# Optimization experiments

Measured on AMD Instinct MI355X. Metric: run time of the kernel, lower is better.

The kernel has to match this reference:

```python
import jax, jax.numpy as jnp
import numpy as np

B, T, C = 4, 2048, 1024
H, D = 16, 64  # n_head, head_dim; H*D == C
EPS = 1e-12


def _l2norm(x):
    # matches torch F.normalize(dim=-1): x / max(||x||_2, eps)
    n = jnp.sqrt(jnp.sum(x * x, axis=-1, keepdims=True))
    return x / jnp.maximum(n, EPS)


def setup_inputs() -> dict:
    key = jax.random.key(0)
    ks = jax.random.split(key, 8)
    s = 0.02
    return {
        "x": jax.random.normal(ks[0], (B, T, C), dtype=jnp.float32),
        "Wq": jax.random.normal(ks[1], (C, C), dtype=jnp.float32) * s,
        "Wk": jax.random.normal(ks[2], (C, C), dtype=jnp.float32) * s,
        "Wv": jax.random.normal(ks[3], (C, C), dtype=jnp.float32) * s,
        "Wbeta": jax.random.normal(ks[4], (H, C), dtype=jnp.float32) * s,
        "bbeta": jnp.zeros((H,), dtype=jnp.float32),
        "Wgate": jax.random.normal(ks[5], (C, C), dtype=jnp.float32) * s,
        "Wo": jax.random.normal(ks[6], (C, C), dtype=jnp.float32) * s,
    }


def _forward(x, Wq, Wk, Wv, Wbeta, bbeta, Wgate, Wo):
    q = (x @ Wq.T).reshape(B, T, H, D)
    k = (x @ Wk.T).reshape(B, T, H, D)
    v = (x @ Wv.T).reshape(B, T, H, D)
    beta = jax.nn.sigmoid(x @ Wbeta.T + bbeta)  # (B,T,H)
    gate = jax.nn.sigmoid(x @ Wgate.T)          # (B,T,C)

    q = _l2norm(q)
    k = _l2norm(k)

    # time-major for scan: (T,B,H,D) / (T,B,H)
    qT = jnp.transpose(q, (1, 0, 2, 3))
    kT = jnp.transpose(k, (1, 0, 2, 3))
    vT = jnp.transpose(v, (1, 0, 2, 3))
    bT = jnp.transpose(beta, (1, 0, 2))

    M0 = jnp.zeros((B, H, D, D), dtype=x.dtype)

    def step(M, inp):
        q_t, k_t, v_t, b_t = inp
        o_t = jnp.einsum('bhdc,bhc->bhd', M, q_t)       # read state with q (pre-update)
        Mk = jnp.einsum('bhdc,bhc->bhd', M, k_t)
        dv = v_t - Mk                                    # delta-rule error
        M = M + b_t[..., None, None] * jnp.einsum('bhd,bhc->bhdc', dv, k_t)
        return M, o_t

    _, oT = jax.lax.scan(step, M0, (qT, kT, vT, bT))     # oT: (T,B,H,D)
    o = jnp.transpose(oT, (1, 0, 2, 3)).reshape(B, T, C)
    return (gate * o) @ Wo.T


def reference(x, Wq, Wk, Wv, Wbeta, bbeta, Wgate, Wo):
    return _forward(x, Wq, Wk, Wv, Wbeta, bbeta, Wgate, Wo)
```

## Files before the change

kernel.cpp:

```cpp
#include <hip/hip_runtime.h>
#include <cstdint>
#include <cstddef>

#define Bz 4
#define Tz 2048
#define Cz 1024
#define Hz 16
#define Dz 64
#define NTOK (Bz*Tz)
#define CHL 32
#define NCH (Tz/CHL)

typedef __attribute__((ext_vector_type(8))) short  short8;
typedef __attribute__((ext_vector_type(4))) float  floatx4;

__device__ __forceinline__ unsigned short f2bf(float x) {
  union { float f; uint32_t u; } a; a.f = x;
  uint32_t r = a.u + 0x7fffu + ((a.u >> 16) & 1u);
  return (unsigned short)(r >> 16);
}
__device__ __forceinline__ float bf2f(unsigned short u) {
  union { uint32_t i; float f; } a; a.i = ((uint32_t)u) << 16; return a.f;
}
__device__ __forceinline__ float sigmoidf_(float z) {
  return 1.0f / (1.0f + __expf(-z));
}

__device__ __forceinline__ void gload_lds16(const void* gptr, void* lptr) {
  __builtin_amdgcn_global_load_lds(
      (const __attribute__((address_space(1))) void*)(uintptr_t)gptr,
      (__attribute__((address_space(3))) void*)(uint32_t)(uintptr_t)lptr,
      16, 0, 0);
}

template<int CTRL>
__device__ __forceinline__ float dpp_addf(float x) {
  int y = __builtin_amdgcn_update_dpp(0, __float_as_int(x), CTRL, 0xF, 0xF, true);
  return x + __int_as_float(y);
}
__device__ __forceinline__ float rowsum16(float x) {
  x = dpp_addf<0xB1>(x);
  x = dpp_addf<0x4E>(x);
  x = dpp_addf<0x124>(x);
  x = dpp_addf<0x128>(x);
  return x;
}

union FragU { uint32_t u[4]; short8 s; };

__global__ __launch_bounds__(256) void cvt_bf16_kernel(const float* __restrict__ in,
                                                       unsigned short* __restrict__ out,
                                                       int n4) {
  int i = blockIdx.x * blockDim.x + threadIdx.x;
  int stride = gridDim.x * blockDim.x;
  const float4* in4 = (const float4*)in;
  ushort4* out4 = (ushort4*)out;
  for (; i < n4; i += stride) {
    float4 f = in4[i];
    ushort4 u;
    u.x = f2bf(f.x); u.y = f2bf(f.y); u.z = f2bf(f.z); u.w = f2bf(f.w);
    out4[i] = u;
  }
}

__global__ __launch_bounds__(256) void cvt_w5_kernel(
    const float* __restrict__ s0, const float* __restrict__ s1,
    const float* __restrict__ s2, const float* __restrict__ s3,
    const float* __restrict__ s4,
    unsigned short* __restrict__ d0, unsigned short* __restrict__ d1,
    unsigned short* __restrict__ d2, unsigned short* __restrict__ d3,
    unsigned short* __restrict__ d4, int n4)
{
  const int w = blockIdx.y;
  const float* s = (w == 0) ? s0 : (w == 1) ? s1 : (w == 2) ? s2 : (w == 3) ? s3 : s4;
  unsigned short* d = (w == 0) ? d0 : (w == 1) ? d1 : (w == 2) ? d2 : (w == 3) ? d3 : d4;
  int i = blockIdx.x * blockDim.x + threadIdx.x;
  if (i < n4) {
    float4 f = ((const float4*)s)[i];
    ushort4 u;
    u.x = f2bf(f.x); u.y = f2bf(f.y); u.z = f2bf(f.z); u.w = f2bf(f.w);
    ((ushort4*)d)[i] = u;
  }
}


#define VM8()  asm volatile("s_waitcnt vmcnt(8)" ::: "memory")
#define VM4()  asm volatile("s_waitcnt vmcnt(4)" ::: "memory")
#define VM0()  asm volatile("s_waitcnt vmcnt(0)" ::: "memory")
#define LGKM0() asm volatile("s_waitcnt lgkmcnt(0)" ::: "memory")
#define BARR() __builtin_amdgcn_s_barrier()

__global__ __launch_bounds__(512, 2) void gemm256_kernel(
    const unsigned short* __restrict__ A,
    const unsigned short* __restrict__ W0, const unsigned short* __restrict__ W1,
    const unsigned short* __restrict__ W2, const unsigned short* __restrict__ W3,
    void* __restrict__ O0, void* __restrict__ O1,
    void* __restrict__ O2, void* __restrict__ O3,
    int M, int N, int K, int nz_sigmoid, int norm_mask, int out_bf16)
{
  __shared__ unsigned short smem[8 * 8192];

  const int gx = gridDim.x, gz = gridDim.z;
  const int nwg = gx * gridDim.y * gz;
  int flat = (blockIdx.z * gridDim.y + blockIdx.y) * gx + blockIdx.x;
  if ((nwg & 7) == 0) flat = (flat & 7) * (nwg >> 3) + (flat >> 3);
  const int xz = gx * gz;
  const int by = flat / xz;
  const int rem = flat - by * xz;
  const int bz = rem / gx;
  const int bx = rem - bz * gx;

  const unsigned short* Bw = (bz == 0) ? W0 : (bz == 1) ? W1 : (bz == 2) ? W2 : W3;
  void* Cw = (bz == 0) ? O0 : (bz == 1) ? O1 : (bz == 2) ? O2 : O3;
  const bool act = (bz == nz_sigmoid);
  const bool donorm = (norm_mask >> bz) & 1;

  const int m0 = by * 256, n0 = bx * 256;
  const int tid = threadIdx.x;
  const int wid = tid >> 6, lane = tid & 63;
  const int wm = wid >> 2, wn = wid & 3;
  const int ml = lane & 15, kq = lane >> 4;

  const unsigned short* Ap = A  + (size_t)m0 * K;
  const unsigned short* Bp = Bw + (size_t)n0 * K;

  const int srow = wid * 16 + (lane >> 2);
  const int ss8  = ((lane & 3) ^ ((lane >> 3) & 3)) * 8;

  const int rs8  = (kq ^ ((ml >> 1) & 3)) * 8;
  const int arow = wm * 128 + ml;
  const int brow = wn * 64 + ml;

  const int NT = K >> 6;
  const int hmax = NT << 2;

  floatx4 acc[8][4];
#pragma unroll
  for (int i = 0; i < 8; ++i)
#pragma unroll
    for (int j = 0; j < 4; ++j) acc[i][j] = floatx4{0.f, 0.f, 0.f, 0.f};

#define STAGE1(hsi) do {                                                      \
    const int ht_ = (hsi) >> 2, hh_ = (hsi) & 3;                              \
    const unsigned short* p_ = (hh_ & 1) ? Bp : Ap;                           \
    const int kb_ = ht_ * 64 + (hh_ >> 1) * 32;                               \
    unsigned short* lb_ = &smem[(((ht_ & 1) << 2) + hh_) * 8192 + wid * 512]; \
    gload_lds16(p_ + (size_t)srow * K + kb_ + ss8, lb_);                      \
    gload_lds16(p_ + (size_t)(128 + srow) * K + kb_ + ss8, lb_ + 4096);       \
  } while (0)

  int hs = 0;
  for (; hs < 6 && hs < hmax; ++hs) STAGE1(hs);
  VM8();
  BARR();

#define LOAD_A(Hb, mh)                                                        \
  _Pragma("unroll") for (int i = 0; i < 4; ++i)                               \
    af[i] = *(const short8*)&Hb[(arow + (mh) * 64 + i * 16) * 32 + rs8];
#define LOAD_B(Hb)                                                            \
  _Pragma("unroll") for (int j = 0; j < 4; ++j)                               \
    bf[j] = *(const short8*)&Hb[(brow + j * 16) * 32 + rs8];
#define MFMA_Q(mh)                                                            \
  __builtin_amdgcn_s_setprio(1);                                              \
  _Pragma("unroll") for (int i = 0; i < 4; ++i)                               \
    _Pragma("unroll") for (int j = 0; j < 4; ++j)                             \
      acc[(mh) * 4 + i][j] = __builtin_amdgcn_mfma_f32_16x16x32_bf16(         \
          af[i], bf[j], acc[(mh) * 4 + i][j], 0, 0, 0);                       \
  __builtin_amdgcn_s_setprio(0);
#define STAGE_NEXT() do { if (hs < hmax) { STAGE1(hs); ++hs; } } while (0)

  short8 af[4], bf[4];
  for (int t = 0; t < NT; ++t) {
    const unsigned short* Ah0 = &smem[(((t & 1) << 2) + 0) * 8192];
    const unsigned short* Bh0 = &smem[(((t & 1) << 2) + 1) * 8192];
    const unsigned short* Ah1 = &smem[(((t & 1) << 2) + 2) * 8192];
    const unsigned short* Bh1 = &smem[(((t & 1) << 2) + 3) * 8192];

    LOAD_A(Ah0, 0); LOAD_B(Bh0);
    STAGE_NEXT();
    BARR(); LGKM0();
    MFMA_Q(0);
    BARR();

    LOAD_A(Ah0, 1);
    STAGE_NEXT();
    BARR(); LGKM0();
    MFMA_Q(1);
    if (t == NT - 1) { VM0(); } else { VM8(); }
    BARR();

    LOAD_A(Ah1, 0); LOAD_B(Bh1);
    STAGE_NEXT();
    BARR(); LGKM0();
    MFMA_Q(0);
    BARR();

    LOAD_A(Ah1, 1);
    STAGE_NEXT();
    BARR(); LGKM0();
    MFMA_Q(1);
    if (t < NT - 2) { VM8(); } else if (t == NT - 2) { VM4(); }
    BARR();
  }

  float scale[8][4];
  if (donorm) {
#pragma unroll
    for (int i = 0; i < 8; ++i) {
#pragma unroll
      for (int r = 0; r < 4; ++r) {
        float ss = 0.f;
#pragma unroll
        for (int j = 0; j < 4; ++j) ss = fmaf(acc[i][j][r], acc[i][j][r], ss);
        ss = rowsum16(ss);
        scale[i][r] = 1.0f / fmaxf(sqrtf(ss), 1e-12f);
      }
    }
  }

  const int row_base = m0 + wm * 128;
  const int col_base = n0 + wn * 64;
#pragma unroll
  for (int i = 0; i < 8; ++i) {
#pragma unroll
    for (int j = 0; j < 4; ++j) {
      const int col = col_base + j * 16 + ml;
#pragma unroll
      for (int r = 0; r < 4; ++r) {
        const int row = row_base + i * 16 + kq * 4 + r;
        float val = acc[i][j][r];
        if (donorm) val *= scale[i][r];
        if (act) val = sigmoidf_(val);
        if (out_bf16) ((unsigned short*)Cw)[(size_t)row * N + col] = f2bf(val);
        else          ((float*)Cw)[(size_t)row * N + col] = val;
      }
    }
  }
}

__global__ __launch_bounds__(256) void beta_kernel(
    const float* __restrict__ x, const float* __restrict__ Wb,
    const float* __restrict__ bb, float* __restrict__ beta_out)
{
  const int n = blockIdx.x;
  const int wid = threadIdx.x >> 6;
  const int lane = threadIdx.x & 63;
  const float* xr = x + (size_t)n * Cz;
  for (int h = wid; h < Hz; h += 4) {
    const float* wr = Wb + (size_t)h * Cz;
    float s = 0.f;
#pragma unroll 4
    for (int i = lane; i < Cz; i += 64) s = fmaf(xr[i], wr[i], s);
#pragma unroll
    for (int ofs = 32; ofs >= 1; ofs >>= 1) s += __shfl_xor(s, ofs);
    if (lane == 0) beta_out[(size_t)n * Hz + h] = sigmoidf_(s + bb[h]);
  }
}

__global__ __launch_bounds__(256) void deltachunk_phase1(
    const unsigned short* __restrict__ qb, const unsigned short* __restrict__ kb,
    const unsigned short* __restrict__ vb, const float* __restrict__ betaf,
    float* __restrict__ of,
    unsigned short* __restrict__ qtb, unsigned short* __restrict__ wbuf,
    unsigned short* __restrict__ ubuf, unsigned short* __restrict__ ktb)
{
  __shared__ unsigned short Kb[32][72], Qb[32][72], Vb[32][72];
  __shared__ float As[32][33];
  __shared__ unsigned short Sb[32][40];
  __shared__ unsigned short Us[32][72], Ws[32][72], Qts[32][72];
  __shared__ float bsh[32];

  const int bid = blockIdx.x;
  const int chain = bid & 63;
  const int chunk = bid >> 6;
  const int b = chain >> 4, h = chain & 15;
  const int tid = threadIdx.x;
  const int wid = tid >> 6, lane = tid & 63;
  const int ml = lane & 15, kq = lane >> 4;

  const size_t tok0 = (size_t)b * Tz + (size_t)chunk * CHL;
  const size_t cb = ((size_t)chain * NCH + chunk) * 2048;

  {
    const int row = tid >> 3, c8 = (tid & 7) * 8;
    const size_t ga = (tok0 + row) * Cz + h * Dz + c8;
    *(uint4*)&Qb[row][c8] = *(const uint4*)&qb[ga];
    *(uint4*)&Kb[row][c8] = *(const uint4*)&kb[ga];
    *(uint4*)&Vb[row][c8] = *(const uint4*)&vb[ga];
  }
  if (tid < 32) bsh[tid] = betaf[(tok0 + tid) * Hz + h];
  __syncthreads();

  {
    const int tr = wid & 1, tc = wid >> 1;
    floatx4 accA = {0.f,0.f,0.f,0.f}, accS = {0.f,0.f,0.f,0.f};
#pragma unroll
    for (int eh = 0; eh < 2; ++eh) {
      short8 ka = *(const short8*)&Kb[tr * 16 + ml][eh * 32 + kq * 8];
      short8 kbf = *(const short8*)&Kb[tc * 16 + ml][eh * 32 + kq * 8];
      short8 qa = *(const short8*)&Qb[tr * 16 + ml][eh * 32 + kq * 8];
      accA = __builtin_amdgcn_mfma_f32_16x16x32_bf16(ka, kbf, accA, 0, 0, 0);
      accS = __builtin_amdgcn_mfma_f32_16x16x32_bf16(qa, kbf, accS, 0, 0, 0);
    }
#pragma unroll
    for (int r = 0; r < 4; ++r) {
      int t = tr * 16 + kq * 4 + r;
      int s = tc * 16 + ml;
      As[t][s] = bsh[t] * accA[r];
      Sb[t][s] = (t > s) ? f2bf(accS[r]) : (unsigned short)0;
    }
  }
  __syncthreads();

  if (tid < 128) {
    const int j = tid;
    float x[32];
    if (j < 64) {
#pragma unroll
      for (int t = 0; t < 32; ++t) x[t] = bsh[t] * bf2f(Vb[t][j]);
    } else {
#pragma unroll
      for (int t = 0; t < 32; ++t) x[t] = bsh[t] * bf2f(Kb[t][j - 64]);
    }
#pragma unroll
    for (int t = 0; t < 31; ++t) {
      float xt = x[t];
#pragma unroll
      for (int s = t + 1; s < 32; ++s) x[s] = fmaf(-As[s][t], xt, x[s]);
    }
    if (j < 64) {
#pragma unroll
      for (int t = 0; t < 32; ++t) Us[t][j] = f2bf(x[t]);
    } else {
#pragma unroll
      for (int t = 0; t < 32; ++t) Ws[t][j - 64] = f2bf(x[t]);
    }
  }
  __syncthreads();

  {
    const int dw = wid * 16 + ml;
    FragU bu, bw;
#pragma unroll
    for (int r = 0; r < 4; ++r) {
      bu.u[r] = (uint32_t)Us[kq * 8 + 2 * r][dw] | ((uint32_t)Us[kq * 8 + 2 * r + 1][dw] << 16);
      bw.u[r] = (uint32_t)Ws[kq * 8 + 2 * r][dw] | ((uint32_t)Ws[kq * 8 + 2 * r + 1][dw] << 16);
    }
    floatx4 accO[2], accQ[2];
#pragma unroll
    for (int tt = 0; tt < 2; ++tt) { accO[tt] = floatx4{0.f,0.f,0.f,0.f}; accQ[tt] = floatx4{0.f,0.f,0.f,0.f}; }
#pragma unroll
    for (int tt = 0; tt < 2; ++tt) {
      short8 sa = *(const short8*)&Sb[tt * 16 + ml][kq * 8];
      accO[tt] = __builtin_amdgcn_mfma_f32_16x16x32_bf16(sa, bu.s, accO[tt], 0, 0, 0);
      accQ[tt] = __builtin_amdgcn_mfma_f32_16x16x32_bf16(sa, bw.s, accQ[tt], 0, 0, 0);
    }
#pragma unroll
    for (int tt = 0; tt < 2; ++tt) {
#pragma unroll
      for (int r = 0; r < 4; ++r) {
        int t = tt * 16 + kq * 4 + r;
        of[(tok0 + t) * Cz + h * Dz + dw] = accO[tt][r];
        Qts[t][dw] = f2bf(bf2f(Qb[t][dw]) - accQ[tt][r]);
      }
    }
  }

  unsigned short ktmp[8];
  {
    const int e = tid >> 2, tq = (tid & 3) * 8;
#pragma unroll
    for (int i2 = 0; i2 < 8; ++i2) ktmp[i2] = Kb[tq + i2][e];
  }
  __syncthreads();

  {
    const int row = tid >> 3, c8 = (tid & 7) * 8;
    const size_t o16 = cb + (size_t)row * 64 + c8;
    *(uint4*)&qtb[o16]  = *(const uint4*)&Qts[row][c8];
    *(uint4*)&wbuf[o16] = *(const uint4*)&Ws[row][c8];
    *(uint4*)&ubuf[o16] = *(const uint4*)&Us[row][c8];
    const int e = tid >> 2, tq = (tid & 3) * 8;
    *(uint4*)&ktb[cb + (size_t)e * 32 + tq] = *(const uint4*)ktmp;
  }
}

__global__ __launch_bounds__(256) void deltachunk_phase2(
    const unsigned short* __restrict__ qtb, const unsigned short* __restrict__ wbuf,
    const unsigned short* __restrict__ ubuf, const unsigned short* __restrict__ ktb,
    float* __restrict__ of)
{
  __shared__ unsigned short Gb[64][72];
  __shared__ unsigned short Kts[64][40];
  __shared__ unsigned short Ub[32][72];
  __shared__ unsigned short Mh[64][72], Ml[64][72];
  __shared__ unsigned short Zh[64][40], Zl[64][40];

  const int chain = blockIdx.x;
  const int b = chain >> 4, h = chain & 15;
  const int tid = threadIdx.x;
  const int wid = tid >> 6, lane = tid & 63;
  const int ml = lane & 15, kq = lane >> 4;
  const int iq = wid >> 1, jq = wid & 1;
  const int dq = wid >> 1, eq = wid & 1;

  for (int i = tid; i < 64 * 72; i += 256) { (&Mh[0][0])[i] = 0; (&Ml[0][0])[i] = 0; }
  floatx4 mAcc[2][2];
#pragma unroll
  for (int a = 0; a < 2; ++a)
#pragma unroll
    for (int e = 0; e < 2; ++e) mAcc[a][e] = floatx4{0.f,0.f,0.f,0.f};

  const int grow = tid >> 3, gc8 = (tid & 7) * 8;
  const int ke = tid >> 2,  kt8 = (tid & 3) * 8;

  {
    const size_t cb = (size_t)chain * NCH * 2048;
    *(uint4*)&Gb[grow][gc8]      = *(const uint4*)&qtb[cb + (size_t)grow * 64 + gc8];
    *(uint4*)&Gb[32 + grow][gc8] = *(const uint4*)&wbuf[cb + (size_t)grow * 64 + gc8];
    *(uint4*)&Ub[grow][gc8]      = *(const uint4*)&ubuf[cb + (size_t)grow * 64 + gc8];
    *(uint4*)&Kts[ke][kt8]       = *(const uint4*)&ktb[cb + (size_t)ke * 32 + kt8];
  }
  __syncthreads();

  for (int c = 0; c < NCH; ++c) {
    const size_t tok0 = (size_t)b * Tz + (size_t)c * CHL;
    float pre[2][2][4];
    if (iq == 0) {
#pragma unroll
      for (int ti = 0; ti < 2; ++ti)
#pragma unroll
        for (int tj = 0; tj < 2; ++tj)
#pragma unroll
          for (int r = 0; r < 4; ++r)
            pre[ti][tj][r] = of[(tok0 + ti * 16 + kq * 4 + r) * Cz + h * Dz + jq * 32 + tj * 16 + ml];
    }
    const int cn = (c + 1 < NCH) ? c + 1 : c;
    const size_t cbn = ((size_t)chain * NCH + cn) * 2048;
    uint4 sq = *(const uint4*)&qtb[cbn + (size_t)grow * 64 + gc8];
    uint4 sw = *(const uint4*)&wbuf[cbn + (size_t)grow * 64 + gc8];
    uint4 su = *(const uint4*)&ubuf[cbn + (size_t)grow * 64 + gc8];
    uint4 sk = *(const uint4*)&ktb[cbn + (size_t)ke * 32 + kt8];

    __syncthreads();

    floatx4 g1[2][2];
#pragma unroll
    for (int ti = 0; ti < 2; ++ti)
#pragma unroll
      for (int tj = 0; tj < 2; ++tj) g1[ti][tj] = floatx4{0.f,0.f,0.f,0.f};
#pragma unroll
    for (int eh = 0; eh < 2; ++eh) {
      short8 afr[2];
      afr[0] = *(const short8*)&Gb[iq * 32 + 0  + ml][eh * 32 + kq * 8];
      afr[1] = *(const short8*)&Gb[iq * 32 + 16 + ml][eh * 32 + kq * 8];
#pragma unroll
      for (int hl = 0; hl < 2; ++hl) {
#pragma unroll
        for (int tj = 0; tj < 2; ++tj) {
          short8 bfr = hl ? *(const short8*)&Ml[jq * 32 + tj * 16 + ml][eh * 32 + kq * 8]
                          : *(const short8*)&Mh[jq * 32 + tj * 16 + ml][eh * 32 + kq * 8];
          g1[0][tj] = __builtin_amdgcn_mfma_f32_16x16x32_bf16(afr[0], bfr, g1[0][tj], 0, 0, 0);
          g1[1][tj] = __builtin_amdgcn_mfma_f32_16x16x32_bf16(afr[1], bfr, g1[1][tj], 0, 0, 0);
        }
      }
    }
    if (iq == 0) {
#pragma unroll
      for (int ti = 0; ti < 2; ++ti)
#pragma unroll
        for (int tj = 0; tj < 2; ++tj)
#pragma unroll
          for (int r = 0; r < 4; ++r)
            of[(tok0 + ti * 16 + kq * 4 + r) * Cz + h * Dz + jq * 32 + tj * 16 + ml] =
                pre[ti][tj][r] + g1[ti][tj][r];
    } else {
#pragma unroll
      for (int ti = 0; ti < 2; ++ti)
#pragma unroll
        for (int tj = 0; tj < 2; ++tj)
#pragma unroll
          for (int r = 0; r < 4; ++r) {
            int t = ti * 16 + kq * 4 + r, d = jq * 32 + tj * 16 + ml;
            float z = bf2f(Ub[t][d]) - g1[ti][tj][r];
            unsigned short zh = f2bf(z);
            Zh[d][t] = zh;
            Zl[d][t] = f2bf(z - bf2f(zh));
          }
    }
    __syncthreads();

    {
      short8 kfr[2];
      kfr[0] = *(const short8*)&Kts[eq * 32 + 0  + ml][kq * 8];
      kfr[1] = *(const short8*)&Kts[eq * 32 + 16 + ml][kq * 8];
#pragma unroll
      for (int hl = 0; hl < 2; ++hl) {
#pragma unroll
        for (int dt = 0; dt < 2; ++dt) {
          short8 afr = hl ? *(const short8*)&Zl[dq * 32 + dt * 16 + ml][kq * 8]
                          : *(const short8*)&Zh[dq * 32 + dt * 16 + ml][kq * 8];
          mAcc[dt][0] = __builtin_amdgcn_mfma_f32_16x16x32_bf16(afr, kfr[0], mAcc[dt][0], 0, 0, 0);
          mAcc[dt][1] = __builtin_amdgcn_mfma_f32_16x16x32_bf16(afr, kfr[1], mAcc[dt][1], 0, 0, 0);
        }
      }
#pragma unroll
      for (int dt = 0; dt < 2; ++dt)
#pragma unroll
        for (int et = 0; et < 2; ++et)
#pragma unroll
          for (int r = 0; r < 4; ++r) {
            int d = dq * 32 + dt * 16 + kq * 4 + r;
            int ec = eq * 32 + et * 16 + ml;
            float mv = mAcc[dt][et][r];
            unsigned short mh = f2bf(mv);
            Mh[d][ec] = mh;
            Ml[d][ec] = f2bf(mv - bf2f(mh));
          }
    }
    __syncthreads();

    *(uint4*)&Gb[grow][gc8]      = sq;
    *(uint4*)&Gb[32 + grow][gc8] = sw;
    *(uint4*)&Ub[grow][gc8]      = su;
    *(uint4*)&Kts[ke][kt8]       = sk;
  }
}

__global__ __launch_bounds__(256) void gate_mul_kernel(
    const unsigned short* __restrict__ gsig, const float* __restrict__ o,
    unsigned short* __restrict__ out, int n4)
{
  int i = blockIdx.x * blockDim.x + threadIdx.x;
  int stride = gridDim.x * blockDim.x;
  const ushort4* g4 = (const ushort4*)gsig;
  const float4* o4 = (const float4*)o;
  ushort4* out4 = (ushort4*)out;
  for (; i < n4; i += stride) {
    ushort4 gv = g4[i];
    float4 ov = o4[i];
    ushort4 u;
    u.x = f2bf(bf2f(gv.x) * ov.x);
    u.y = f2bf(bf2f(gv.y) * ov.y);
    u.z = f2bf(bf2f(gv.z) * ov.z);
    u.w = f2bf(bf2f(gv.w) * ov.w);
    out4[i] = u;
  }
}

extern "C" void kernel_launch(void* const* d_in, const int* in_sizes, int n_in,
                              void* d_out, int out_size, void* d_ws, size_t ws_size,
                              hipStream_t stream) {
  const float* x     = (const float*)d_in[0];
  const float* Wq    = (const float*)d_in[1];
  const float* Wk    = (const float*)d_in[2];
  const float* Wv    = (const float*)d_in[3];
  const float* Wbeta = (const float*)d_in[4];
  const float* bbeta = (const float*)d_in[5];
  const float* Wgate = (const float*)d_in[6];
  const float* Wo    = (const float*)d_in[7];
  float* out = (float*)d_out;

  char* ws = (char*)d_ws;
  size_t off = 0;
  auto alloc = [&](size_t bytes) -> char* {
    char* p = ws + off;
    off += (bytes + 255) & ~(size_t)255;
    return p;
  };
  unsigned short* xb  = (unsigned short*)alloc((size_t)NTOK * Cz * 2);
  unsigned short* Wqb = (unsigned short*)alloc((size_t)Cz * Cz * 2);
  unsigned short* Wkb = (unsigned short*)alloc((size_t)Cz * Cz * 2);
  unsigned short* Wvb = (unsigned short*)alloc((size_t)Cz * Cz * 2);
  unsigned short* Wgb = (unsigned short*)alloc((size_t)Cz * Cz * 2);
  unsigned short* Wob = (unsigned short*)alloc((size_t)Cz * Cz * 2);
  unsigned short* qb  = (unsigned short*)alloc((size_t)NTOK * Cz * 2);
  unsigned short* kb  = (unsigned short*)alloc((size_t)NTOK * Cz * 2);
  unsigned short* vb  = (unsigned short*)alloc((size_t)NTOK * Cz * 2);
  unsigned short* gb  = (unsigned short*)alloc((size_t)NTOK * Cz * 2);
  float* of    = (float*)alloc((size_t)NTOK * Cz * 4);
  float* betaf = (float*)alloc((size_t)NTOK * Hz * 4);
  unsigned short* qtb  = (unsigned short*)alloc((size_t)64 * NCH * 2048 * 2);
  unsigned short* wbuf = (unsigned short*)alloc((size_t)64 * NCH * 2048 * 2);
  unsigned short* ubuf = (unsigned short*)alloc((size_t)64 * NCH * 2048 * 2);
  unsigned short* ktb  = (unsigned short*)alloc((size_t)64 * NCH * 2048 * 2);
  unsigned short* ab = xb;

  const int n4x = NTOK * Cz / 4;
  const int n4w = Cz * Cz / 4;

  cvt_bf16_kernel<<<dim3(1024), dim3(256), 0, stream>>>(x, xb, n4x);
  cvt_w5_kernel<<<dim3(n4w / 256, 5), dim3(256), 0, stream>>>(
      Wq, Wk, Wv, Wgate, Wo, Wqb, Wkb, Wvb, Wgb, Wob, n4w);

  gemm256_kernel<<<dim3(Cz / 256, NTOK / 256, 4), dim3(512), 0, stream>>>(
      xb, Wqb, Wkb, Wvb, Wgb, qb, kb, vb, gb, NTOK, Cz, Cz, 3, 3, 1);

  beta_kernel<<<dim3(NTOK), dim3(256), 0, stream>>>(x, Wbeta, bbeta, betaf);

  deltachunk_phase1<<<dim3(64 * NCH), dim3(256), 0, stream>>>(
      qb, kb, vb, betaf, of, qtb, wbuf, ubuf, ktb);
  deltachunk_phase2<<<dim3(Bz * Hz), dim3(256), 0, stream>>>(qtb, wbuf, ubuf, ktb, of);

  gate_mul_kernel<<<dim3(1024), dim3(256), 0, stream>>>(gb, of, ab, n4x);

  gemm256_kernel<<<dim3(Cz / 256, NTOK / 256, 1), dim3(512), 0, stream>>>(
      ab, Wob, Wob, Wob, Wob, out, out, out, out, NTOK, Cz, Cz, -1, 0, 0);
}
```

Baseline: 417.5 us.

## Double-buffer delta-rule chunk scan and split waves between output and state update

The sequential chunk-scan kernel now double-buffers the chunk inputs and the state matrix in LDS, so each chunk needs one barrier instead of three. Waves are specialized: half emit the output and stage the next chunk's data, while the other half compute the state update. Those update waves pass the residual fragments between lanes with ds_bpermute instead of going through LDS, and use packed bf16 conversion for the hi/lo split. Phase 1 now writes U transposed to fit the new layout. The cost is more LDS, unbalanced work between the two wave groups, and extra register pressure on a kernel that runs only one block per chain.

```diff
diff --git a/kernel.cpp b/kernel.cpp
--- a/kernel.cpp
+++ b/kernel.cpp
@@ -24,6 +24,17 @@
 }
 __device__ __forceinline__ float sigmoidf_(float z) {
   return 1.0f / (1.0f + __expf(-z));
+}
+__device__ __forceinline__ uint32_t cvtpk_bf16(float a, float b) {
+  uint32_t d;
+  asm volatile("v_cvt_pk_bf16_f32 %0, %1, %2" : "=v"(d) : "v"(a), "v"(b));
+  return d;
+}
+__device__ __forceinline__ float lo16f(uint32_t u) {
+  union { uint32_t i; float f; } a; a.i = u << 16; return a.f;
+}
+__device__ __forceinline__ float hi16f(uint32_t u) {
+  union { uint32_t i; float f; } a; a.i = u & 0xffff0000u; return a.f;
 }
 
 __device__ __forceinline__ void gload_lds16(const void* gptr, void* lptr) {
@@ -83,7 +94,6 @@
   }
 }
 
-
 #define VM8()  asm volatile("s_waitcnt vmcnt(8)" ::: "memory")
 #define VM4()  asm volatile("s_waitcnt vmcnt(4)" ::: "memory")
 #define VM0()  asm volatile("s_waitcnt vmcnt(0)" ::: "memory")
@@ -126,7 +136,6 @@
 
   const int srow = wid * 16 + (lane >> 2);
   const int ss8  = ((lane & 3) ^ ((lane >> 3) & 3)) * 8;
-
   const int rs8  = (kq ^ ((ml >> 1) & 3)) * 8;
   const int arow = wm * 128 + ml;
   const int brow = wn * 64 + ml;
@@ -257,6 +266,7 @@
   }
 }
 
+
 __global__ __launch_bounds__(256) void deltachunk_phase1(
     const unsigned short* __restrict__ qb, const unsigned short* __restrict__ kb,
     const unsigned short* __restrict__ vb, const float* __restrict__ betaf,
@@ -366,11 +376,11 @@
     }
   }
 
-  unsigned short ktmp[8];
+  unsigned short ktmp[8], utmp[8];
   {
     const int e = tid >> 2, tq = (tid & 3) * 8;
 #pragma unroll
-    for (int i2 = 0; i2 < 8; ++i2) ktmp[i2] = Kb[tq + i2][e];
+    for (int i2 = 0; i2 < 8; ++i2) { ktmp[i2] = Kb[tq + i2][e]; utmp[i2] = Us[tq + i2][e]; }
   }
   __syncthreads();
 
@@ -379,22 +389,21 @@
     const size_t o16 = cb + (size_t)row * 64 + c8;
     *(uint4*)&qtb[o16]  = *(const uint4*)&Qts[row][c8];
     *(uint4*)&wbuf[o16] = *(const uint4*)&Ws[row][c8];
-    *(uint4*)&ubuf[o16] = *(const uint4*)&Us[row][c8];
     const int e = tid >> 2, tq = (tid & 3) * 8;
-    *(uint4*)&ktb[cb + (size_t)e * 32 + tq] = *(const uint4*)ktmp;
-  }
-}
-
-__global__ __launch_bounds__(256) void deltachunk_phase2(
+    *(uint4*)&ktb[cb + (size_t)e * 32 + tq]  = *(const uint4*)ktmp;
+    *(uint4*)&ubuf[cb + (size_t)e * 32 + tq] = *(const uint4*)utmp;
+  }
+}
+
+__global__ __launch_bounds__(256, 1) void deltachunk_phase2(
     const unsigned short* __restrict__ qtb, const unsigned short* __restrict__ wbuf,
     const unsigned short* __restrict__ ubuf, const unsigned short* __restrict__ ktb,
     float* __restrict__ of)
 {
-  __shared__ unsigned short Gb[64][72];
-  __shared__ unsigned short Kts[64][40];
-  __shared__ unsigned short Ub[32][72];
-  __shared__ unsigned short Mh[64][72], Ml[64][72];
-  __shared__ unsigned short Zh[64][40], Zl[64][40];
+  __shared__ unsigned short Gb[2][64][72];
+  __shared__ unsigned short Ub[2][64][40];
+  __shared__ unsigned short Kts[2][64][40];
+  __shared__ unsigned short Mh[2][64][72], Ml[2][64][72];
 
   const int chain = blockIdx.x;
   const int b = chain >> 4, h = chain & 15;
@@ -402,47 +411,71 @@
   const int wid = tid >> 6, lane = tid & 63;
   const int ml = lane & 15, kq = lane >> 4;
   const int iq = wid >> 1, jq = wid & 1;
-  const int dq = wid >> 1, eq = wid & 1;
-
-  for (int i = tid; i < 64 * 72; i += 256) { (&Mh[0][0])[i] = 0; (&Ml[0][0])[i] = 0; }
-  floatx4 mAcc[2][2];
-#pragma unroll
-  for (int a = 0; a < 2; ++a)
-#pragma unroll
-    for (int e = 0; e < 2; ++e) mAcc[a][e] = floatx4{0.f,0.f,0.f,0.f};
-
-  const int grow = tid >> 3, gc8 = (tid & 7) * 8;
-  const int ke = tid >> 2,  kt8 = (tid & 3) * 8;
-
-  {
-    const size_t cb = (size_t)chain * NCH * 2048;
-    *(uint4*)&Gb[grow][gc8]      = *(const uint4*)&qtb[cb + (size_t)grow * 64 + gc8];
-    *(uint4*)&Gb[32 + grow][gc8] = *(const uint4*)&wbuf[cb + (size_t)grow * 64 + gc8];
-    *(uint4*)&Ub[grow][gc8]      = *(const uint4*)&ubuf[cb + (size_t)grow * 64 + gc8];
-    *(uint4*)&Kts[ke][kt8]       = *(const uint4*)&ktb[cb + (size_t)ke * 32 + kt8];
+
+  for (int i = tid; i < 64 * 72; i += 256) { (&Mh[0][0][0])[i] = 0; (&Ml[0][0][0])[i] = 0; }
+
+  const int g_row = tid >> 2;
+  const int g_c0  = (tid & 3) * 16;
+  const int k_e   = tid >> 1;
+  const int k_c0  = (tid & 1) * 16;
+
+  const size_t cbase = (size_t)chain * NCH * 2048;
+
+  float pre[2][2][4];
+  if (iq == 0) {
+#pragma unroll
+    for (int u = 0; u < 2; ++u) {
+      *(uint4*)&Gb[0][g_row][g_c0 + 8*u]    = *(const uint4*)&qtb[cbase + (size_t)g_row * 64 + g_c0 + 8*u];
+      *(uint4*)&Gb[0][32 + g_row][g_c0 + 8*u] = *(const uint4*)&wbuf[cbase + (size_t)g_row * 64 + g_c0 + 8*u];
+      *(uint4*)&Ub[0][k_e][k_c0 + 8*u]      = *(const uint4*)&ubuf[cbase + (size_t)k_e * 32 + k_c0 + 8*u];
+      *(uint4*)&Kts[0][k_e][k_c0 + 8*u]     = *(const uint4*)&ktb[cbase + (size_t)k_e * 32 + k_c0 + 8*u];
+    }
+    const size_t t0 = (size_t)b * Tz;
+#pragma unroll
+    for (int ti = 0; ti < 2; ++ti)
+#pragma unroll
+      for (int tj = 0; tj < 2; ++tj)
+#pragma unroll
+        for (int r = 0; r < 4; ++r)
+          pre[ti][tj][r] = of[(t0 + ti * 16 + kq * 4 + r) * Cz + h * Dz + jq * 32 + tj * 16 + ml];
   }
   __syncthreads();
 
+  const int idxA = ((lane & 15) + 16 * ((2 * kq + 0) & 3)) * 4;
+  const int idxB = ((lane & 15) + 16 * ((2 * kq + 1) & 3)) * 4;
+  const bool hiKq = (kq >= 2);
+
+  floatx4 mAcc[4][2];
+#pragma unroll
+  for (int a = 0; a < 4; ++a) { mAcc[a][0] = floatx4{0.f,0.f,0.f,0.f}; mAcc[a][1] = floatx4{0.f,0.f,0.f,0.f}; }
+
+  int cbuf = 0;
   for (int c = 0; c < NCH; ++c) {
+    const int nbuf = cbuf ^ 1;
+    const int mr = c & 1, mw = mr ^ 1;
     const size_t tok0 = (size_t)b * Tz + (size_t)c * CHL;
-    float pre[2][2][4];
+
+    uint4 sq[2], sw[2], su[2], sk[2];
+    float preN[2][2][4];
+    const int cn = (c + 1 < NCH) ? c + 1 : c;
     if (iq == 0) {
+      const size_t cbn = cbase + (size_t)cn * 2048;
+#pragma unroll
+      for (int u = 0; u < 2; ++u) {
+        sq[u] = *(const uint4*)&qtb[cbn + (size_t)g_row * 64 + g_c0 + 8*u];
+        sw[u] = *(const uint4*)&wbuf[cbn + (size_t)g_row * 64 + g_c0 + 8*u];
+        su[u] = *(const uint4*)&ubuf[cbn + (size_t)k_e * 32 + k_c0 + 8*u];
+        sk[u] = *(const uint4*)&ktb[cbn + (size_t)k_e * 32 + k_c0 + 8*u];
+      }
+      const size_t tkn = (size_t)b * Tz + (size_t)cn * CHL;
 #pragma unroll
       for (int ti = 0; ti < 2; ++ti)
 #pragma unroll
         for (int tj = 0; tj < 2; ++tj)
 #pragma unroll
           for (int r = 0; r < 4; ++r)
-            pre[ti][tj][r] = of[(tok0 + ti * 16 + kq * 4 + r) * Cz + h * Dz + jq * 32 + tj * 16 + ml];
-    }
-    const int cn = (c + 1 < NCH) ? c + 1 : c;
-    const size_t cbn = ((size_t)chain * NCH + cn) * 2048;
-    uint4 sq = *(const uint4*)&qtb[cbn + (size_t)grow * 64 + gc8];
-    uint4 sw = *(const uint4*)&wbuf[cbn + (size_t)grow * 64 + gc8];
-    uint4 su = *(const uint4*)&ubuf[cbn + (size_t)grow * 64 + gc8];
-    uint4 sk = *(const uint4*)&ktb[cbn + (size_t)ke * 32 + kt8];
-
-    __syncthreads();
+            preN[ti][tj][r] = of[(tkn + ti * 16 + kq * 4 + r) * Cz + h * Dz + jq * 32 + tj * 16 + ml];
+    }
 
     floatx4 g1[2][2];
 #pragma unroll
@@ -451,20 +484,20 @@
       for (int tj = 0; tj < 2; ++tj) g1[ti][tj] = floatx4{0.f,0.f,0.f,0.f};
 #pragma unroll
     for (int eh = 0; eh < 2; ++eh) {
-      short8 afr[2];
-      afr[0] = *(const short8*)&Gb[iq * 32 + 0  + ml][eh * 32 + kq * 8];
-      afr[1] = *(const short8*)&Gb[iq * 32 + 16 + ml][eh * 32 + kq * 8];
+      short8 afr0 = *(const short8*)&Gb[cbuf][iq * 32 + 0  + ml][eh * 32 + kq * 8];
+      short8 afr1 = *(const short8*)&Gb[cbuf][iq * 32 + 16 + ml][eh * 32 + kq * 8];
 #pragma unroll
       for (int hl = 0; hl < 2; ++hl) {
 #pragma unroll
         for (int tj = 0; tj < 2; ++tj) {
-          short8 bfr = hl ? *(const short8*)&Ml[jq * 32 + tj * 16 + ml][eh * 32 + kq * 8]
-                          : *(const short8*)&Mh[jq * 32 + tj * 16 + ml][eh * 32 + kq * 8];
-          g1[0][tj] = __builtin_amdgcn_mfma_f32_16x16x32_bf16(afr[0], bfr, g1[0][tj], 0, 0, 0);
-          g1[1][tj] = __builtin_amdgcn_mfma_f32_16x16x32_bf16(afr[1], bfr, g1[1][tj], 0, 0, 0);
+          short8 bfr = hl ? *(const short8*)&Ml[mr][jq * 32 + tj * 16 + ml][eh * 32 + kq * 8]
+                          : *(const short8*)&Mh[mr][jq * 32 + tj * 16 + ml][eh * 32 + kq * 8];
+          g1[0][tj] = __builtin_amdgcn_mfma_f32_16x16x32_bf16(afr0, bfr, g1[0][tj], 0, 0, 0);
+          g1[1][tj] = __builtin_amdgcn_mfma_f32_16x16x32_bf16(afr1, bfr, g1[1][tj], 0, 0, 0);
         }
       }
     }
+
     if (iq == 0) {
 #pragma unroll
       for (int ti = 0; ti < 2; ++ti)
@@ -474,56 +507,80 @@
           for (int r = 0; r < 4; ++r)
             of[(tok0 + ti * 16 + kq * 4 + r) * Cz + h * Dz + jq * 32 + tj * 16 + ml] =
                 pre[ti][tj][r] + g1[ti][tj][r];
+#pragma unroll
+      for (int u = 0; u < 2; ++u) {
+        *(uint4*)&Gb[nbuf][g_row][g_c0 + 8*u]    = sq[u];
+        *(uint4*)&Gb[nbuf][32 + g_row][g_c0 + 8*u] = sw[u];
+        *(uint4*)&Ub[nbuf][k_e][k_c0 + 8*u]      = su[u];
+        *(uint4*)&Kts[nbuf][k_e][k_c0 + 8*u]     = sk[u];
+      }
+#pragma unroll
+      for (int ti = 0; ti < 2; ++ti)
+#pragma unroll
+        for (int tj = 0; tj < 2; ++tj)
+#pragma unroll
+          for (int r = 0; r < 4; ++r) pre[ti][tj][r] = preN[ti][tj][r];
     } else {
-#pragma unroll
-      for (int ti = 0; ti < 2; ++ti)
-#pragma unroll
-        for (int tj = 0; tj < 2; ++tj)
-#pragma unroll
-          for (int r = 0; r < 4; ++r) {
-            int t = ti * 16 + kq * 4 + r, d = jq * 32 + tj * 16 + ml;
-            float z = bf2f(Ub[t][d]) - g1[ti][tj][r];
-            unsigned short zh = f2bf(z);
-            Zh[d][t] = zh;
-            Zl[d][t] = f2bf(z - bf2f(zh));
-          }
+      uint32_t pkh[2][2][2], pkl[2][2][2];
+#pragma unroll
+      for (int ti = 0; ti < 2; ++ti) {
+#pragma unroll
+        for (int tj = 0; tj < 2; ++tj) {
+          const int d = jq * 32 + tj * 16 + ml;
+          ushort4 uu = *(const ushort4*)&Ub[cbuf][d][ti * 16 + kq * 4];
+          float z0 = bf2f(uu.x) - g1[ti][tj][0];
+          float z1 = bf2f(uu.y) - g1[ti][tj][1];
+          float z2 = bf2f(uu.z) - g1[ti][tj][2];
+          float z3 = bf2f(uu.w) - g1[ti][tj][3];
+          uint32_t h01 = cvtpk_bf16(z0, z1), h23 = cvtpk_bf16(z2, z3);
+          pkh[ti][tj][0] = h01; pkh[ti][tj][1] = h23;
+          pkl[ti][tj][0] = cvtpk_bf16(z0 - lo16f(h01), z1 - hi16f(h01));
+          pkl[ti][tj][1] = cvtpk_bf16(z2 - lo16f(h23), z3 - hi16f(h23));
+        }
+      }
+      FragU zh[2], zl[2];
+#pragma unroll
+      for (int tj = 0; tj < 2; ++tj) {
+#pragma unroll
+        for (int s = 0; s < 4; ++s) {
+          const int idx = (s < 2) ? idxA : idxB;
+          const int rp = s & 1;
+          int v0 = __builtin_amdgcn_ds_bpermute(idx, (int)pkh[0][tj][rp]);
+          int v1 = __builtin_amdgcn_ds_bpermute(idx, (int)pkh[1][tj][rp]);
+          zh[tj].u[s] = hiKq ? (uint32_t)v1 : (uint32_t)v0;
+          int w0 = __builtin_amdgcn_ds_bpermute(idx, (int)pkl[0][tj][rp]);
+          int w1 = __builtin_amdgcn_ds_bpermute(idx, (int)pkl[1][tj][rp]);
+          zl[tj].u[s] = hiKq ? (uint32_t)w1 : (uint32_t)w0;
+        }
+      }
+#pragma unroll
+      for (int et = 0; et < 4; ++et) {
+        short8 kfr = *(const short8*)&Kts[cbuf][et * 16 + ml][kq * 8];
+#pragma unroll
+        for (int tj = 0; tj < 2; ++tj) {
+          mAcc[et][tj] = __builtin_amdgcn_mfma_f32_16x16x32_bf16(kfr, zh[tj].s, mAcc[et][tj], 0, 0, 0);
+          mAcc[et][tj] = __builtin_amdgcn_mfma_f32_16x16x32_bf16(kfr, zl[tj].s, mAcc[et][tj], 0, 0, 0);
+        }
+      }
+#pragma unroll
+      for (int et = 0; et < 4; ++et) {
+#pragma unroll
+        for (int tj = 0; tj < 2; ++tj) {
+          const int d = jq * 32 + tj * 16 + ml;
+          float m0 = mAcc[et][tj][0], m1 = mAcc[et][tj][1];
+          float m2 = mAcc[et][tj][2], m3 = mAcc[et][tj][3];
+          uint32_t h01 = cvtpk_bf16(m0, m1), h23 = cvtpk_bf16(m2, m3);
+          uint32_t l01 = cvtpk_bf16(m0 - lo16f(h01), m1 - hi16f(h01));
+          uint32_t l23 = cvtpk_bf16(m2 - lo16f(h23), m3 - hi16f(h23));
+          *(uint32_t*)&Mh[mw][d][et * 16 + kq * 4]     = h01;
+          *(uint32_t*)&Mh[mw][d][et * 16 + kq * 4 + 2] = h23;
+          *(uint32_t*)&Ml[mw][d][et * 16 + kq * 4]     = l01;
+          *(uint32_t*)&Ml[mw][d][et * 16 + kq * 4 + 2] = l23;
+        }
+      }
     }
     __syncthreads();
-
-    {
-      short8 kfr[2];
-      kfr[0] = *(const short8*)&Kts[eq * 32 + 0  + ml][kq * 8];
-      kfr[1] = *(const short8*)&Kts[eq * 32 + 16 + ml][kq * 8];
-#pragma unroll
-      for (int hl = 0; hl < 2; ++hl) {
-#pragma unroll
-        for (int dt = 0; dt < 2; ++dt) {
-          short8 afr = hl ? *(const short8*)&Zl[dq * 32 + dt * 16 + ml][kq * 8]
-                          : *(const short8*)&Zh[dq * 32 + dt * 16 + ml][kq * 8];
-          mAcc[dt][0] = __builtin_amdgcn_mfma_f32_16x16x32_bf16(afr, kfr[0], mAcc[dt][0], 0, 0, 0);
-          mAcc[dt][1] = __builtin_amdgcn_mfma_f32_16x16x32_bf16(afr, kfr[1], mAcc[dt][1], 0, 0, 0);
-        }
-      }
-#pragma unroll
-      for (int dt = 0; dt < 2; ++dt)
-#pragma unroll
-        for (int et = 0; et < 2; ++et)
-#pragma unroll
-          for (int r = 0; r < 4; ++r) {
-            int d = dq * 32 + dt * 16 + kq * 4 + r;
-            int ec = eq * 32 + et * 16 + ml;
-            float mv = mAcc[dt][et][r];
-            unsigned short mh = f2bf(mv);
-            Mh[d][ec] = mh;
-            Ml[d][ec] = f2bf(mv - bf2f(mh));
-          }
-    }
-    __syncthreads();
-
-    *(uint4*)&Gb[grow][gc8]      = sq;
-    *(uint4*)&Gb[32 + grow][gc8] = sw;
-    *(uint4*)&Ub[grow][gc8]      = su;
-    *(uint4*)&Kts[ke][kt8]       = sk;
+    cbuf ^= 1;
   }
 }
 
```

New measurement: 411.6 us. About the same (-1.4%).
